# Optimization experiments

Hardware: AMD Instinct MI355X
Metric: run time of the kernel (lower is better)

Reference implementation:

```python
import jax, jax.numpy as jnp
import numpy as np

COMMITMENT_COST = 0.25

def _l2norm(v, axis=-1, eps=1e-12):
    # matches F.normalize(p=2): v / max(||v||, eps)
    n = jnp.sqrt(jnp.sum(v * v, axis=axis, keepdims=True))
    return v / jnp.maximum(n, eps)

def setup_inputs() -> dict:
    key = jax.random.key(0)
    k1, k2 = jax.random.split(key)
    N, D, K = 131072, 64, 2048
    x = jax.random.normal(k1, (N, D), dtype=jnp.float32)
    embeddings = jax.random.normal(k2, (K, D), dtype=jnp.float32)
    return {"x": x, "embeddings": embeddings}

def reference(x, embeddings):
    # x: [N, D] latents; embeddings: [K, D] codebook
    xn = _l2norm(x, axis=-1)                 # [N, D]
    en = _l2norm(embeddings, axis=-1)        # [K, D]
    # squared euclidean distances: ||xn||^2 + ||en||^2 - 2 xn.en
    d = (jnp.sum(xn * xn, axis=-1, keepdims=True)
         + jnp.sum(en * en, axis=-1)[None, :]
         - 2.0 * jnp.einsum('nd,kd->nk', xn, en))   # [N, K]
    idx = jnp.argmin(d, axis=1)              # [N] int
    quantized = en[idx]                      # [N, D] (already unit-norm; re-normalizing is idempotent but matches quantize())
    quantized = _l2norm(quantized, axis=-1)
    q_latent_loss = jnp.mean((quantized - jax.lax.stop_gradient(xn)) ** 2)
    e_latent_loss = jnp.mean((xn - jax.lax.stop_gradient(quantized)) ** 2)
    loss = q_latent_loss + COMMITMENT_COST * e_latent_loss
    # straight-through estimator
    quantized_st = xn + jax.lax.stop_gradient(quantized - xn)
    return quantized_st, loss, idx
```

## Files before the change

### kernel.cpp

```cpp
#include <hip/hip_runtime.h>
#include <math.h>
#include <stdint.h>


#define D 64
#define EPS 1e-12f
#define WPB 4
#define RG 2
#define RPW (RG * 16)
#define RPB (WPB * RPW)
#define CAP 832
#define MARGIN 0.010f

typedef short bf16x8 __attribute__((ext_vector_type(8)));
typedef float f32x4 __attribute__((ext_vector_type(4)));

__device__ __forceinline__ uint32_t f2bf(float f) {
    uint32_t u = __builtin_bit_cast(uint32_t, f);
    return (u + 0x7FFFu + ((u >> 16) & 1u)) >> 16;
}
__device__ __forceinline__ int xsw(int row, int d) {
    return row * 64 + ((((d >> 2) ^ (row & 7)) << 2) | (d & 3));
}

__global__ __launch_bounds__(256) void vq_norm_emb(const float* __restrict__ emb,
                                                   float* __restrict__ en,
                                                   float* __restrict__ en2,
                                                   int K) {
    int wave = (int)((blockIdx.x * blockDim.x + threadIdx.x) >> 6);
    int lane = threadIdx.x & 63;
    if (wave >= K) return;
    float v = emb[(size_t)wave * D + lane];
    float s = v * v;
    #pragma unroll
    for (int m = 32; m >= 1; m >>= 1) s += __shfl_xor(s, m, 64);
    float e = v / fmaxf(sqrtf(s), EPS);
    float s2 = e * e;
    #pragma unroll
    for (int m = 32; m >= 1; m >>= 1) s2 += __shfl_xor(s2, m, 64);
    en[(size_t)wave * D + lane] = e;
    if (lane == 0) en2[wave] = s2;
}

__global__ __launch_bounds__(256) void vq_build_frags(const float* __restrict__ en,
                                                      uint32_t* __restrict__ frags,
                                                      int K) {
    int t = (int)(blockIdx.x * blockDim.x + threadIdx.x);
    int tile = t >> 6, lane = t & 63;
    if (tile >= K / 16) return;
    int code = tile * 16 + (lane & 15);
    int dbase = (lane >> 4) * 8;
    #pragma unroll
    for (int h = 0; h < 2; ++h) {
        const float* p = en + (size_t)code * D + h * 32 + dbase;
        uint4 u;
        u.x = f2bf(p[0]) | (f2bf(p[1]) << 16);
        u.y = f2bf(p[2]) | (f2bf(p[3]) << 16);
        u.z = f2bf(p[4]) | (f2bf(p[5]) << 16);
        u.w = f2bf(p[6]) | (f2bf(p[7]) << 16);
        *(uint4*)(frags + ((size_t)(tile * 2 + h) * 64 + lane) * 4) = u;
    }
}

__global__ __launch_bounds__(256, 4) void vq_main(const float* __restrict__ x,
                                                  const float* __restrict__ en,
                                                  const float* __restrict__ en2g,
                                                  const uint32_t* __restrict__ frags,
                                                  float* __restrict__ out_q,
                                                  float* __restrict__ out_idx,
                                                  double* __restrict__ partials,
                                                  int N, int K) {
    __shared__ float xn[RPB * 64];
    __shared__ uint16_t cand[WPB][CAP];
    __shared__ int candcnt[WPB];
    __shared__ unsigned long long keys[RPB];
    __shared__ double red[WPB];

    const int tid = (int)threadIdx.x;
    const int w = tid >> 6, lane = tid & 63;
    const int rowbase = (int)blockIdx.x * RPB;
    const int NT = K / 16;

    for (int r = 0; r < RPW; ++r) {
        int rb = w * RPW + r;
        float v = x[(size_t)(rowbase + rb) * D + lane];
        float s = v * v;
        #pragma unroll
        for (int m = 32; m >= 1; m >>= 1) s += __shfl_xor(s, m, 64);
        xn[xsw(rb, lane)] = v / fmaxf(sqrtf(s), EPS);
    }
    if (lane == 0) candcnt[w] = 0;
    if (lane < RPW) keys[w * RPW + lane] = ~0ull;

    bf16x8 bfr[RG][2];
    #pragma unroll
    for (int g = 0; g < RG; ++g)
        #pragma unroll
        for (int h = 0; h < 2; ++h) {
            int row = w * RPW + g * 16 + (lane & 15);
            int db = h * 32 + ((lane >> 4) * 8);
            union { uint32_t u[4]; bf16x8 v; } cvt;
            #pragma unroll
            for (int j = 0; j < 4; ++j)
                cvt.u[j] = f2bf(xn[xsw(row, db + 2 * j)]) |
                           (f2bf(xn[xsw(row, db + 2 * j + 1)]) << 16);
            bfr[g][h] = cvt.v;
        }

    float runmax[RG];
    #pragma unroll
    for (int g = 0; g < RG; ++g) runmax[g] = -3.0e38f;
    const f32x4 zero4 = {0.f, 0.f, 0.f, 0.f};

    for (int t = 0; t < NT; ++t) {
        bf16x8 a0 = *(const bf16x8*)(frags + ((size_t)(t * 2 + 0) * 64 + lane) * 4);
        bf16x8 a1 = *(const bf16x8*)(frags + ((size_t)(t * 2 + 1) * 64 + lane) * 4);
        int cb = t * 16 + ((lane >> 4) << 2);
        f32x4 acc[RG];
        #pragma unroll
        for (int g = 0; g < RG; ++g) {
            acc[g] = __builtin_amdgcn_mfma_f32_16x16x32_bf16(a0, bfr[g][0], zero4, 0, 0, 0);
            acc[g] = __builtin_amdgcn_mfma_f32_16x16x32_bf16(a1, bfr[g][1], acc[g], 0, 0, 0);
        }
        #pragma unroll
        for (int g = 0; g < RG; ++g) {
            float m4 = fmaxf(fmaxf(acc[g][0], acc[g][1]), fmaxf(acc[g][2], acc[g][3]));
            float rm = fmaxf(m4, __shfl_xor(m4, 16, 64));
            rm = fmaxf(rm, __shfl_xor(rm, 32, 64));
            runmax[g] = fmaxf(runmax[g], rm);
            float tau = runmax[g] - MARGIN;
            if (__any(m4 >= tau)) {
                int rloc = g * 16 + (lane & 15);
                #pragma unroll
                for (int q = 0; q < 4; ++q) {
                    if (acc[g][q] >= tau) {
                        int k = cb + q;
                        int slot = atomicAdd(&candcnt[w], 1);
                        if (slot < CAP) {
                            cand[w][slot] = (uint16_t)((k << 5) | rloc);
                        } else {
                            const float* ev = en + (size_t)k * D;
                            float dot = 0.f;
                            #pragma unroll
                            for (int d0 = 0; d0 < D; ++d0)
                                dot = fmaf(xn[xsw(w * RPW + rloc, d0)], ev[d0], dot);
                            float R = fmaf(-0.5f, en2g[k], dot);
                            uint32_t fb = __builtin_bit_cast(uint32_t, -R);
                            uint32_t ord = (fb & 0x80000000u) ? ~fb : (fb | 0x80000000u);
                            atomicMin(&keys[w * RPW + rloc],
                                      ((unsigned long long)ord << 32) | (uint32_t)k);
                        }
                    }
                }
            }
        }
        if ((t & 15) == 15) __syncthreads();
    }

    int cnt = candcnt[w];
    cnt = cnt < CAP ? cnt : CAP;
    for (int base = 0; base < cnt; base += 64) {
        int i = base + lane;
        if (i < cnt) {
            uint32_t e = cand[w][i];
            int k = (int)(e >> 5), rloc = (int)(e & 31u);
            const float* ev = en + (size_t)k * D;
            float dot = 0.f;
            #pragma unroll
            for (int d0 = 0; d0 < D; ++d0)
                dot = fmaf(xn[xsw(w * RPW + rloc, d0)], ev[d0], dot);
            float R = fmaf(-0.5f, en2g[k], dot);
            uint32_t fb = __builtin_bit_cast(uint32_t, -R);
            uint32_t ord = (fb & 0x80000000u) ? ~fb : (fb | 0x80000000u);
            atomicMin(&keys[w * RPW + rloc],
                      ((unsigned long long)ord << 32) | (uint32_t)k);
        }
    }

    float ls = 0.f;
    for (int r = 0; r < RPW; ++r) {
        int rb = w * RPW + r;
        int k = (int)(keys[rb] & 0x7FFull);
        float rn = fmaxf(sqrtf(en2g[k]), EPS);
        float q = en[(size_t)k * D + lane] / rn;
        float a = xn[xsw(rb, lane)];
        float dx = q - a;
        ls = fmaf(dx, dx, ls);
        out_q[(size_t)(rowbase + rb) * D + lane] = a + dx;
    }
    if (lane < RPW) out_idx[rowbase + w * RPW + lane] =
        (float)(int)(keys[w * RPW + lane] & 0x7FFull);
    #pragma unroll
    for (int m = 32; m >= 1; m >>= 1) ls += __shfl_xor(ls, m, 64);
    if (lane == 0) red[w] = (double)ls;
    __syncthreads();
    if (tid == 0) {
        double s = 0.0;
        #pragma unroll
        for (int i = 0; i < WPB; ++i) s += red[i];
        partials[blockIdx.x] = s;
    }
}

__global__ __launch_bounds__(512) void vq_finalize(const double* __restrict__ partials,
                                                   int nb, float* __restrict__ loss_out,
                                                   int N) {
    __shared__ double red[512];
    int t = (int)threadIdx.x;
    double s = 0.0;
    for (int i = t; i < nb; i += 512) s += partials[i];
    red[t] = s;
    __syncthreads();
    #pragma unroll
    for (int off = 256; off >= 1; off >>= 1) {
        if (t < off) red[t] += red[t + off];
        __syncthreads();
    }
    if (t == 0) {
        double mean = red[0] / ((double)N * (double)D);
        loss_out[0] = (float)(mean * 1.25);
    }
}

extern "C" void kernel_launch(void* const* d_in, const int* in_sizes, int n_in,
                              void* d_out, int out_size, void* d_ws, size_t ws_size,
                              hipStream_t stream) {
    const float* x   = (const float*)d_in[0];
    const float* emb = (const float*)d_in[1];
    int N = in_sizes[0] / D;
    int K = in_sizes[1] / D;

    float* out      = (float*)d_out;
    float* out_q    = out;
    float* loss_out = out + (size_t)N * D;
    float* out_idx  = out + (size_t)N * D + 1;

    char* ws = (char*)d_ws;
    double*   partials = (double*)ws;
    float*    en2      = (float*)(ws + 8192);
    float*    en       = (float*)(ws + 16384);
    uint32_t* frags    = (uint32_t*)(ws + 540672);

    vq_norm_emb<<<(K + 3) / 4, 256, 0, stream>>>(emb, en, en2, K);
    vq_build_frags<<<(K / 16 * 64 + 255) / 256, 256, 0, stream>>>(en, frags, K);

    int nbB = N / RPB;
    vq_main<<<nbB, 256, 0, stream>>>(x, en, en2, frags, out_q, out_idx,
                                     partials, N, K);
    vq_finalize<<<1, 512, 0, stream>>>(partials, nbB, loss_out, N);
}
```

Before: 195.5 us.

## Fuse prep kernels, drop finalize via atomic loss, software-pipeline codebook fragment loads

Merges the embedding normalization and bf16 fragment building into a single prep kernel that stages rows in shared memory. It also replaces the partials buffer and finalize kernel with a float atomicAdd of each block's scaled loss, which also zeroes the loss in prep. The main loop is unrolled by two with register double-buffering, so the next tile's fragments load while the current tile is scored. This cuts two kernel launches and hides global-load latency, at the cost of extra registers and a float atomic reduction whose summation order is nondeterministic.

```diff
diff --git a/kernel.cpp b/kernel.cpp
--- a/kernel.cpp
+++ b/kernel.cpp
@@ -23,42 +23,43 @@
     return row * 64 + ((((d >> 2) ^ (row & 7)) << 2) | (d & 3));
 }
 
-__global__ __launch_bounds__(256) void vq_norm_emb(const float* __restrict__ emb,
-                                                   float* __restrict__ en,
-                                                   float* __restrict__ en2,
-                                                   int K) {
-    int wave = (int)((blockIdx.x * blockDim.x + threadIdx.x) >> 6);
-    int lane = threadIdx.x & 63;
-    if (wave >= K) return;
-    float v = emb[(size_t)wave * D + lane];
-    float s = v * v;
-    #pragma unroll
-    for (int m = 32; m >= 1; m >>= 1) s += __shfl_xor(s, m, 64);
-    float e = v / fmaxf(sqrtf(s), EPS);
-    float s2 = e * e;
-    #pragma unroll
-    for (int m = 32; m >= 1; m >>= 1) s2 += __shfl_xor(s2, m, 64);
-    en[(size_t)wave * D + lane] = e;
-    if (lane == 0) en2[wave] = s2;
-}
-
-__global__ __launch_bounds__(256) void vq_build_frags(const float* __restrict__ en,
-                                                      uint32_t* __restrict__ frags,
-                                                      int K) {
-    int t = (int)(blockIdx.x * blockDim.x + threadIdx.x);
-    int tile = t >> 6, lane = t & 63;
-    if (tile >= K / 16) return;
-    int code = tile * 16 + (lane & 15);
-    int dbase = (lane >> 4) * 8;
-    #pragma unroll
-    for (int h = 0; h < 2; ++h) {
-        const float* p = en + (size_t)code * D + h * 32 + dbase;
-        uint4 u;
-        u.x = f2bf(p[0]) | (f2bf(p[1]) << 16);
-        u.y = f2bf(p[2]) | (f2bf(p[3]) << 16);
-        u.z = f2bf(p[4]) | (f2bf(p[5]) << 16);
-        u.w = f2bf(p[6]) | (f2bf(p[7]) << 16);
-        *(uint4*)(frags + ((size_t)(tile * 2 + h) * 64 + lane) * 4) = u;
+__global__ __launch_bounds__(1024) void vq_prep(const float* __restrict__ emb,
+                                                float* __restrict__ en,
+                                                float* __restrict__ en2,
+                                                uint32_t* __restrict__ frags,
+                                                float* __restrict__ loss_out,
+                                                int K) {
+    __shared__ float sh[16][64];
+    int w = (int)(threadIdx.x >> 6), lane = (int)(threadIdx.x & 63);
+    int tile = (int)blockIdx.x;
+    int row = tile * 16 + w;
+    if (row < K) {
+        float v = emb[(size_t)row * D + lane];
+        float s = v * v;
+        #pragma unroll
+        for (int m = 32; m >= 1; m >>= 1) s += __shfl_xor(s, m, 64);
+        float e = v / fmaxf(sqrtf(s), EPS);
+        float s2 = e * e;
+        #pragma unroll
+        for (int m = 32; m >= 1; m >>= 1) s2 += __shfl_xor(s2, m, 64);
+        en[(size_t)row * D + lane] = e;
+        if (lane == 0) en2[row] = s2;
+        sh[w][lane] = e;
+    }
+    if (blockIdx.x == 0 && threadIdx.x == 0) loss_out[0] = 0.f;
+    __syncthreads();
+    if (w == 0) {
+        int cl = lane & 15, dbase = (lane >> 4) * 8;
+        #pragma unroll
+        for (int h = 0; h < 2; ++h) {
+            const float* p = &sh[cl][h * 32 + dbase];
+            uint4 u;
+            u.x = f2bf(p[0]) | (f2bf(p[1]) << 16);
+            u.y = f2bf(p[2]) | (f2bf(p[3]) << 16);
+            u.z = f2bf(p[4]) | (f2bf(p[5]) << 16);
+            u.w = f2bf(p[6]) | (f2bf(p[7]) << 16);
+            *(uint4*)(frags + ((size_t)(tile * 2 + h) * 64 + lane) * 4) = u;
+        }
     }
 }
 
@@ -68,7 +69,7 @@
                                                   const uint32_t* __restrict__ frags,
                                                   float* __restrict__ out_q,
                                                   float* __restrict__ out_idx,
-                                                  double* __restrict__ partials,
+                                                  float* __restrict__ loss_out,
                                                   int N, int K) {
     __shared__ float xn[RPB * 64];
     __shared__ uint16_t cand[WPB][CAP];
@@ -80,6 +81,7 @@
     const int w = tid >> 6, lane = tid & 63;
     const int rowbase = (int)blockIdx.x * RPB;
     const int NT = K / 16;
+    const int lq = (lane >> 4) << 2;
 
     for (int r = 0; r < RPW; ++r) {
         int rb = w * RPW + r;
@@ -112,15 +114,13 @@
     for (int g = 0; g < RG; ++g) runmax[g] = -3.0e38f;
     const f32x4 zero4 = {0.f, 0.f, 0.f, 0.f};
 
-    for (int t = 0; t < NT; ++t) {
-        bf16x8 a0 = *(const bf16x8*)(frags + ((size_t)(t * 2 + 0) * 64 + lane) * 4);
-        bf16x8 a1 = *(const bf16x8*)(frags + ((size_t)(t * 2 + 1) * 64 + lane) * 4);
-        int cb = t * 16 + ((lane >> 4) << 2);
+    auto score = [&](int T, bf16x8 A0, bf16x8 A1) {
+        int cb = T * 16 + lq;
         f32x4 acc[RG];
         #pragma unroll
         for (int g = 0; g < RG; ++g) {
-            acc[g] = __builtin_amdgcn_mfma_f32_16x16x32_bf16(a0, bfr[g][0], zero4, 0, 0, 0);
-            acc[g] = __builtin_amdgcn_mfma_f32_16x16x32_bf16(a1, bfr[g][1], acc[g], 0, 0, 0);
+            acc[g] = __builtin_amdgcn_mfma_f32_16x16x32_bf16(A0, bfr[g][0], zero4, 0, 0, 0);
+            acc[g] = __builtin_amdgcn_mfma_f32_16x16x32_bf16(A1, bfr[g][1], acc[g], 0, 0, 0);
         }
         #pragma unroll
         for (int g = 0; g < RG; ++g) {
@@ -154,7 +154,17 @@
                 }
             }
         }
-        if ((t & 15) == 15) __syncthreads();
+    };
+
+    const bf16x8* p = (const bf16x8*)frags + lane;
+    bf16x8 A0 = p[0], A1 = p[64];
+    for (int t = 0; t < NT; t += 2) {
+        bf16x8 B0 = p[128], B1 = p[192];
+        score(t, A0, A1);
+        if (t + 2 < NT) { A0 = p[256]; A1 = p[320]; }
+        score(t + 1, B0, B1);
+        p += 256;
+        if (((t + 1) & 15) == 15) __syncthreads();
     }
 
     int cnt = candcnt[w];
@@ -198,27 +208,7 @@
         double s = 0.0;
         #pragma unroll
         for (int i = 0; i < WPB; ++i) s += red[i];
-        partials[blockIdx.x] = s;
-    }
-}
-
-__global__ __launch_bounds__(512) void vq_finalize(const double* __restrict__ partials,
-                                                   int nb, float* __restrict__ loss_out,
-                                                   int N) {
-    __shared__ double red[512];
-    int t = (int)threadIdx.x;
-    double s = 0.0;
-    for (int i = t; i < nb; i += 512) s += partials[i];
-    red[t] = s;
-    __syncthreads();
-    #pragma unroll
-    for (int off = 256; off >= 1; off >>= 1) {
-        if (t < off) red[t] += red[t + off];
-        __syncthreads();
-    }
-    if (t == 0) {
-        double mean = red[0] / ((double)N * (double)D);
-        loss_out[0] = (float)(mean * 1.25);
+        atomicAdd(loss_out, (float)(s * (1.25 / ((double)N * (double)D))));
     }
 }
 
@@ -236,16 +226,11 @@
     float* out_idx  = out + (size_t)N * D + 1;
 
     char* ws = (char*)d_ws;
-    double*   partials = (double*)ws;
-    float*    en2      = (float*)(ws + 8192);
-    float*    en       = (float*)(ws + 16384);
-    uint32_t* frags    = (uint32_t*)(ws + 540672);
-
-    vq_norm_emb<<<(K + 3) / 4, 256, 0, stream>>>(emb, en, en2, K);
-    vq_build_frags<<<(K / 16 * 64 + 255) / 256, 256, 0, stream>>>(en, frags, K);
-
-    int nbB = N / RPB;
-    vq_main<<<nbB, 256, 0, stream>>>(x, en, en2, frags, out_q, out_idx,
-                                     partials, N, K);
-    vq_finalize<<<1, 512, 0, stream>>>(partials, nbB, loss_out, N);
-}
+    float*    en2   = (float*)(ws + 8192);
+    float*    en    = (float*)(ws + 16384);
+    uint32_t* frags = (uint32_t*)(ws + 540672);
+
+    vq_prep<<<K / 16, 1024, 0, stream>>>(emb, en, en2, frags, loss_out, K);
+    vq_main<<<N / RPB, 256, 0, stream>>>(x, en, en2, frags, out_q, out_idx,
+                                         loss_out, N, K);
+}
```

Measured after the change: 184.2 us. 5.8% less time.
